# Optimization experiments

Measured on AMD Instinct MI355X. Metric: run time of the kernel, lower is better.

Reference implementation:

```python
import jax, jax.numpy as jnp
import numpy as np

N, L, D = 256, 512, 512


def _attention(x, W_in, W_out, apply_tanh):
    # x: [N, L, D]; 'general' attention: project query, score against context (=x)
    q = jnp.einsum('bld,ed->ble', x, W_in)          # [N, L, D]
    scores = jnp.einsum('bld,bmd->blm', q, x)       # [N, L, L]
    w = jax.nn.softmax(scores, axis=-1)             # softmax over keys
    mix = jnp.einsum('blm,bmd->bld', w, x)          # [N, L, D]
    comb = jnp.concatenate([mix, q], axis=-1)       # [N, L, 2D]
    out = jnp.einsum('blc,dc->bld', comb, W_out)    # Linear(2D, D), no bias
    return jnp.tanh(out) if apply_tanh else out


def setup_inputs() -> dict:
    key = jax.random.key(0)
    k1, k2, k3, k4, k5 = jax.random.split(key, 5)
    s = 0.02
    return {
        'embeddings': jax.random.normal(k1, (N, L, D), dtype=jnp.float32),
        'W_in1': jax.random.normal(k2, (D, D), dtype=jnp.float32) * s,
        'W_out1': jax.random.normal(k3, (D, 2 * D), dtype=jnp.float32) * s,
        'W_in2': jax.random.normal(k4, (D, D), dtype=jnp.float32) * s,
        'W_out2': jax.random.normal(k5, (D, 2 * D), dtype=jnp.float32) * s,
    }


def reference(embeddings, W_in1, W_out1, W_in2, W_out2):
    x = _attention(embeddings, W_in1, W_out1, apply_tanh=True)   # block 1 (tanh)
    x = _attention(x, W_in2, W_out2, apply_tanh=False)           # block 2 (no tanh)
    # transpose(1,2) + avg_pool1d over full length == mean over L
    pooled = jnp.mean(x, axis=1)                                  # [N, D]
    return pooled.reshape(pooled.shape[0], -1, 1, 1)              # [N, D, 1, 1]
```

## Files before the change

### kernel.cpp

```cpp
#include <hip/hip_runtime.h>
#include <cstdint>
#include <cstddef>

typedef uint16_t u16;
typedef __attribute__((ext_vector_type(8))) short bf16x8;
typedef __attribute__((ext_vector_type(4))) float f32x4;
typedef __attribute__((ext_vector_type(4))) uint16_t u16x4;

#define GLOBAL_AS(p) (const __attribute__((address_space(1))) void*)(p)
#define LDS_AS(p)    (__attribute__((address_space(3))) void*)(p)

__device__ __forceinline__ u16 f2b(float f){
  uint32_t u = __float_as_uint(f);
  u += 0x7fff + ((u >> 16) & 1);
  return (u16)(u >> 16);
}
__device__ __forceinline__ float b2f(u16 h){
  return __uint_as_float(((uint32_t)h) << 16);
}

__global__ void cvt_bf16_kernel(const float* __restrict__ src, u16* __restrict__ dst, int n){
  int i = (blockIdx.x * 256 + threadIdx.x) * 4;
  if (i >= n) return;
  float4 f = *(const float4*)(src + i);
  u16x4 o; o.x = f2b(f.x); o.y = f2b(f.y); o.z = f2b(f.z); o.w = f2b(f.w);
  *(u16x4*)(dst + i) = o;
}

__global__ void cvtT_kernel(const float* __restrict__ src, u16* __restrict__ x, u16* __restrict__ xT){
  __shared__ u16 tile[64][68];
  size_t b = blockIdx.y;
  int t = blockIdx.x;
  int r0 = (t >> 3) * 64, c0 = (t & 7) * 64;
  const float* s = src + b * 262144;
  u16* dx = x + b * 262144;
  u16* dT = xT + b * 262144;
  int tx = threadIdx.x & 63, ty = threadIdx.x >> 6;
  #pragma unroll
  for (int k = 0; k < 16; k++){
    int r = ty * 16 + k;
    u16 v = f2b(s[(size_t)(r0 + r) * 512 + c0 + tx]);
    dx[(size_t)(r0 + r) * 512 + c0 + tx] = v;
    tile[r][tx] = v;
  }
  __syncthreads();
  #pragma unroll
  for (int k = 0; k < 16; k++){
    int c = ty * 16 + k;
    dT[(size_t)(c0 + c) * 512 + r0 + tx] = tile[tx][c];
  }
}

__global__ void transpose512_kernel(const u16* __restrict__ src, u16* __restrict__ dst){
  __shared__ u16 tile[64][68];
  size_t b = blockIdx.y;
  int t = blockIdx.x;
  int r0 = (t >> 3) * 64, c0 = (t & 7) * 64;
  const u16* s = src + b * 262144;
  u16* d = dst + b * 262144;
  int tx = threadIdx.x & 63, ty = threadIdx.x >> 6;
  #pragma unroll
  for (int k = 0; k < 16; k++){
    int r = ty * 16 + k;
    tile[r][tx] = s[(size_t)(r0 + r) * 512 + c0 + tx];
  }
  __syncthreads();
  #pragma unroll
  for (int k = 0; k < 16; k++){
    int c = ty * 16 + k;
    d[(size_t)(c0 + c) * 512 + r0 + tx] = tile[tx][c];
  }
}

__global__ __launch_bounds__(512, 2) void attn_kernel(
    const u16* __restrict__ q, const u16* __restrict__ x, const u16* __restrict__ xT,
    u16* __restrict__ mix, int batPerXcd)
{
  __shared__ __align__(16) u16 U[64 * 520];
  __shared__ __align__(16) u16 Bx[512 * 32];
  __shared__ float stats[2][64][8];
  const int64_t E = 262144;
  int id = blockIdx.x;
  int tile = (id >> 3) & 7;
  int64_t bat = (int64_t)(id & 7) * batPerXcd + (id >> 6);
  q += bat * E; x += bat * E; xT += bat * E; mix += bat * E;
  int m0 = tile * 64;
  int tid = threadIdx.x, lane = tid & 63, w = tid >> 6;
  int fr = lane & 15, qd = lane >> 4, fq = qd * 8;

  #pragma unroll
  for (int c = 0; c < 8; c++){
    int id2 = c * 512 + tid;
    int row = id2 >> 6, cb = id2 & 63;
    *(bf16x8*)&U[row * 520 + cb * 8] =
        *(const bf16x8*)(q + (size_t)(m0 + row) * 512 + cb * 8);
  }

  f32x4 acc[4][4];
  #pragma unroll
  for (int i = 0; i < 4; i++)
    #pragma unroll
    for (int j = 0; j < 4; j++) acc[i][j] = (f32x4){0.f, 0.f, 0.f, 0.f};

  for (int k0 = 0; k0 < 512; k0 += 32){
    #pragma unroll
    for (int s = 0; s < 4; s++){
      const u16* g = x + (size_t)(s * 128 + (tid >> 2)) * 512 + k0 + (tid & 3) * 8;
      __builtin_amdgcn_global_load_lds(GLOBAL_AS(g), LDS_AS(&Bx[s * 4096 + tid * 8]), 16, 0, 0);
    }
    __syncthreads();
    bf16x8 af[4], bfr[4];
    #pragma unroll
    for (int i = 0; i < 4; i++) af[i]  = *(const bf16x8*)&U[(i * 16 + fr) * 520 + k0 + fq];
    #pragma unroll
    for (int j = 0; j < 4; j++) bfr[j] = *(const bf16x8*)&Bx[(w * 64 + j * 16 + fr) * 32 + fq];
    #pragma unroll
    for (int i = 0; i < 4; i++)
      #pragma unroll
      for (int j = 0; j < 4; j++)
        acc[i][j] = __builtin_amdgcn_mfma_f32_16x16x32_bf16(af[i], bfr[j], acc[i][j], 0, 0, 0);
    __syncthreads();
  }

  float inv[4][4];
  #pragma unroll
  for (int i = 0; i < 4; i++)
    #pragma unroll
    for (int r = 0; r < 4; r++){
      float m = acc[i][0][r];
      #pragma unroll
      for (int j = 1; j < 4; j++) m = fmaxf(m, acc[i][j][r]);
      #pragma unroll
      for (int o = 1; o <= 8; o <<= 1) m = fmaxf(m, __shfl_xor(m, o));
      if (fr == 0) stats[0][i * 16 + qd * 4 + r][w] = m;
    }
  __syncthreads();
  #pragma unroll
  for (int i = 0; i < 4; i++)
    #pragma unroll
    for (int r = 0; r < 4; r++){
      int row = i * 16 + qd * 4 + r;
      float m = stats[0][row][0];
      #pragma unroll
      for (int t = 1; t < 8; t++) m = fmaxf(m, stats[0][row][t]);
      float s = 0.f;
      #pragma unroll
      for (int j = 0; j < 4; j++){
        float e = __expf(acc[i][j][r] - m);
        acc[i][j][r] = e; s += e;
      }
      #pragma unroll
      for (int o = 1; o <= 8; o <<= 1) s += __shfl_xor(s, o);
      if (fr == 0) stats[1][row][w] = s;
    }
  __syncthreads();
  #pragma unroll
  for (int i = 0; i < 4; i++)
    #pragma unroll
    for (int r = 0; r < 4; r++){
      int row = i * 16 + qd * 4 + r;
      float s = stats[1][row][0];
      #pragma unroll
      for (int t = 1; t < 8; t++) s += stats[1][row][t];
      inv[i][r] = 1.0f / s;
    }
  #pragma unroll
  for (int i = 0; i < 4; i++)
    #pragma unroll
    for (int r = 0; r < 4; r++)
      #pragma unroll
      for (int j = 0; j < 4; j++){
        int row = i * 16 + qd * 4 + r;
        int col = w * 64 + j * 16 + fr;
        uint32_t mine = f2b(acc[i][j][r] * inv[i][r]);
        uint32_t oth = (uint32_t)__shfl_xor((int)mine, 1);
        if (!(fr & 1)) *(uint32_t*)&U[row * 520 + col] = mine | (oth << 16);
      }
  __syncthreads();

  #pragma unroll
  for (int i = 0; i < 4; i++)
    #pragma unroll
    for (int j = 0; j < 4; j++) acc[i][j] = (f32x4){0.f, 0.f, 0.f, 0.f};
  for (int k0 = 0; k0 < 512; k0 += 32){
    #pragma unroll
    for (int s = 0; s < 4; s++){
      const u16* g = xT + (size_t)(s * 128 + (tid >> 2)) * 512 + k0 + (tid & 3) * 8;
      __builtin_amdgcn_global_load_lds(GLOBAL_AS(g), LDS_AS(&Bx[s * 4096 + tid * 8]), 16, 0, 0);
    }
    __syncthreads();
    bf16x8 af[4], bfr[4];
    #pragma unroll
    for (int i = 0; i < 4; i++) af[i]  = *(const bf16x8*)&U[(i * 16 + fr) * 520 + k0 + fq];
    #pragma unroll
    for (int j = 0; j < 4; j++) bfr[j] = *(const bf16x8*)&Bx[(w * 64 + j * 16 + fr) * 32 + fq];
    #pragma unroll
    for (int i = 0; i < 4; i++)
      #pragma unroll
      for (int j = 0; j < 4; j++)
        acc[i][j] = __builtin_amdgcn_mfma_f32_16x16x32_bf16(af[i], bfr[j], acc[i][j], 0, 0, 0);
    __syncthreads();
  }
  #pragma unroll
  for (int i = 0; i < 4; i++)
    #pragma unroll
    for (int j = 0; j < 4; j++)
      #pragma unroll
      for (int r = 0; r < 4; r++)
        mix[(size_t)(m0 + i * 16 + qd * 4 + r) * 512 + w * 64 + j * 16 + fr] =
            f2b(acc[i][j][r]);
}

template<bool SPLIT, bool TANH, bool POOL, typename CT>
__global__ __launch_bounds__(256, 2) void gemm_bt_kernel(
    const u16* __restrict__ A0, const u16* __restrict__ A1,
    const u16* __restrict__ B, CT* __restrict__ C,
    int K, int ldb, int64_t aBatch, int64_t bBatch, int64_t cBatch,
    float* __restrict__ poolOut, int b0)
{
  __shared__ __align__(16) u16 As[128 * 32];
  __shared__ __align__(16) u16 Bs[128 * 32];
  int64_t bat = blockIdx.y;
  int m0 = (blockIdx.x & 3) * 128, n0 = (blockIdx.x >> 2) * 128;
  A0 += bat * aBatch;
  if (SPLIT) A1 += bat * aBatch;
  B += bat * bBatch;
  if (!POOL) C += bat * cBatch;
  int tid = threadIdx.x, lane = tid & 63;
  int w = tid >> 6;
  int wm = (w >> 1) * 64, wn = (w & 1) * 64;
  f32x4 acc[4][4];
  #pragma unroll
  for (int i = 0; i < 4; i++)
    #pragma unroll
    for (int j = 0; j < 4; j++) acc[i][j] = (f32x4){0.f, 0.f, 0.f, 0.f};

  int sRow = tid >> 2, sCol = (tid & 3) * 8;
  int fr = lane & 15, fq = (lane >> 4) * 8;

  for (int k0 = 0; k0 < K; k0 += 32){
    const u16* Ap = A0; int kk = k0;
    if (SPLIT && k0 >= 512){ Ap = A1; kk = k0 - 512; }
    const u16* ga = Ap + (size_t)(m0 + sRow) * 512 + kk + sCol;
    const u16* gb = B  + (size_t)(n0 + sRow) * ldb + k0 + sCol;
    __builtin_amdgcn_global_load_lds(GLOBAL_AS(ga),                    LDS_AS(&As[tid * 8]),        16, 0, 0);
    __builtin_amdgcn_global_load_lds(GLOBAL_AS(ga + (size_t)64 * 512), LDS_AS(&As[2048 + tid * 8]), 16, 0, 0);
    __builtin_amdgcn_global_load_lds(GLOBAL_AS(gb),                    LDS_AS(&Bs[tid * 8]),        16, 0, 0);
    __builtin_amdgcn_global_load_lds(GLOBAL_AS(gb + (size_t)64 * ldb), LDS_AS(&Bs[2048 + tid * 8]), 16, 0, 0);
    __syncthreads();
    bf16x8 af[4], bfr[4];
    #pragma unroll
    for (int i = 0; i < 4; i++) af[i]  = *(const bf16x8*)&As[(wm + i * 16 + fr) * 32 + fq];
    #pragma unroll
    for (int j = 0; j < 4; j++) bfr[j] = *(const bf16x8*)&Bs[(wn + j * 16 + fr) * 32 + fq];
    #pragma unroll
    for (int i = 0; i < 4; i++)
      #pragma unroll
      for (int j = 0; j < 4; j++)
        acc[i][j] = __builtin_amdgcn_mfma_f32_16x16x32_bf16(af[i], bfr[j], acc[i][j], 0, 0, 0);
    __syncthreads();
  }

  if constexpr (POOL){
    #pragma unroll
    for (int j = 0; j < 4; j++){
      float p = 0.f;
      #pragma unroll
      for (int i = 0; i < 4; i++)
        #pragma unroll
        for (int r = 0; r < 4; r++) p += acc[i][j][r];
      p += __shfl_xor(p, 16);
      p += __shfl_xor(p, 32);
      if (lane < 16){
        int col = n0 + wn + j * 16 + lane;
        atomicAdd(poolOut + ((size_t)(b0) + bat) * 512 + col, p * (1.0f / 512.0f));
      }
    }
  } else {
    int cq = (lane >> 4) * 4, cc = lane & 15;
    #pragma unroll
    for (int i = 0; i < 4; i++){
      #pragma unroll
      for (int j = 0; j < 4; j++){
        #pragma unroll
        for (int r = 0; r < 4; r++){
          int row = m0 + wm + i * 16 + cq + r;
          int col = n0 + wn + j * 16 + cc;
          float v = acc[i][j][r];
          if (TANH) v = tanhf(v);
          if constexpr (sizeof(CT) == 4) C[(size_t)row * 512 + col] = v;
          else                           C[(size_t)row * 512 + col] = f2b(v);
        }
      }
    }
  }
}

extern "C" void kernel_launch(void* const* d_in, const int* in_sizes, int n_in,
                              void* d_out, int out_size, void* d_ws, size_t ws_size,
                              hipStream_t stream) {
  const float* emb   = (const float*)d_in[0];
  const float* Win1  = (const float*)d_in[1];
  const float* Wout1 = (const float*)d_in[2];
  const float* Win2  = (const float*)d_in[3];
  const float* Wout2 = (const float*)d_in[4];
  float* out = (float*)d_out;

  int CB = 256;
  while (CB > 8 && (4ull << 20) + (size_t)CB * (5ull * 524288ull) > ws_size) CB >>= 1;
  const int64_t E = 262144;

  char* wsb = (char*)d_ws;
  u16* Win1b  = (u16*)wsb;
  u16* Wout1b = Win1b + 262144;
  u16* Win2b  = Wout1b + 524288;
  u16* Wout2b = Win2b + 262144;
  u16* base = (u16*)(wsb + (4 << 20));
  u16* Ar = base;
  u16* Br = base + (size_t)CB * E;
  u16* Cr = base + 2 * (size_t)CB * E;
  u16* Dr = base + 3 * (size_t)CB * E;
  u16* Fr = base + 4 * (size_t)CB * E;

  hipMemsetAsync(d_out, 0, (size_t)out_size * sizeof(float), stream);

  cvt_bf16_kernel<<<256, 256, 0, stream>>>(Win1,  Win1b,  262144);
  cvt_bf16_kernel<<<512, 256, 0, stream>>>(Wout1, Wout1b, 524288);
  cvt_bf16_kernel<<<256, 256, 0, stream>>>(Win2,  Win2b,  262144);
  cvt_bf16_kernel<<<512, 256, 0, stream>>>(Wout2, Wout2b, 524288);

  dim3 gg(16, CB);
  dim3 gt(64, CB);
  int nAttnBlocks = CB * 8;
  int batPerXcd = CB / 8;

  for (int c = 0; c < 256 / CB; c++){
    const float* embc = emb + (size_t)c * CB * 262144;
    int b0 = c * CB;

    cvtT_kernel<<<gt, 256, 0, stream>>>(embc, Ar, Cr);
    gemm_bt_kernel<false,false,false,u16><<<gg, 256, 0, stream>>>(
        Ar, nullptr, Win1b, Br, 512, 512, E, 0, E, nullptr, 0);
    attn_kernel<<<nAttnBlocks, 512, 0, stream>>>(Br, Ar, Cr, Fr, batPerXcd);
    gemm_bt_kernel<true,true,false,u16><<<gg, 256, 0, stream>>>(
        Fr, Br, Wout1b, Dr, 1024, 1024, E, 0, E, nullptr, 0);

    transpose512_kernel<<<gt, 256, 0, stream>>>(Dr, Cr);
    gemm_bt_kernel<false,false,false,u16><<<gg, 256, 0, stream>>>(
        Dr, nullptr, Win2b, Ar, 512, 512, E, 0, E, nullptr, 0);
    attn_kernel<<<nAttnBlocks, 512, 0, stream>>>(Ar, Dr, Cr, Fr, batPerXcd);
    gemm_bt_kernel<true,false,true,u16><<<gg, 256, 0, stream>>>(
        Fr, Ar, Wout2b, (u16*)nullptr, 1024, 1024, E, 0, 0, out, b0);
  }
}
```

Baseline: 1.850 ms.

## Double-buffer LDS tiles to overlap global loads with MFMA in attention and GEMM

```diff
diff --git a/kernel.cpp b/kernel.cpp
--- a/kernel.cpp
+++ b/kernel.cpp
@@ -9,6 +9,17 @@
 
 #define GLOBAL_AS(p) (const __attribute__((address_space(1))) void*)(p)
 #define LDS_AS(p)    (__attribute__((address_space(3))) void*)(p)
+
+__device__ __forceinline__ void wait_all_bar(){
+  asm volatile("s_waitcnt vmcnt(0) lgkmcnt(0)" ::: "memory");
+  __builtin_amdgcn_s_barrier();
+  asm volatile("" ::: "memory");
+}
+__device__ __forceinline__ void wait_lgkm_bar(){
+  asm volatile("s_waitcnt lgkmcnt(0)" ::: "memory");
+  __builtin_amdgcn_s_barrier();
+  asm volatile("" ::: "memory");
+}
 
 __device__ __forceinline__ u16 f2b(float f){
   uint32_t u = __float_as_uint(f);
@@ -77,7 +88,7 @@
     u16* __restrict__ mix, int batPerXcd)
 {
   __shared__ __align__(16) u16 U[64 * 520];
-  __shared__ __align__(16) u16 Bx[512 * 32];
+  __shared__ __align__(16) u16 Bx[2][512 * 32];
   __shared__ float stats[2][64][8];
   const int64_t E = 262144;
   int id = blockIdx.x;
@@ -88,6 +99,16 @@
   int tid = threadIdx.x, lane = tid & 63, w = tid >> 6;
   int fr = lane & 15, qd = lane >> 4, fq = qd * 8;
 
+  auto stage = [&](const u16* __restrict__ src, int buf, int k0){
+    #pragma unroll
+    for (int s = 0; s < 4; s++){
+      const u16* g = src + (size_t)(s * 128 + (tid >> 2)) * 512 + k0 + (tid & 3) * 8;
+      __builtin_amdgcn_global_load_lds(GLOBAL_AS(g), LDS_AS(&Bx[buf][s * 4096 + tid * 8]), 16, 0, 0);
+    }
+  };
+
+  stage(x, 0, 0);
+
   #pragma unroll
   for (int c = 0; c < 8; c++){
     int id2 = c * 512 + tid;
@@ -102,25 +123,25 @@
     #pragma unroll
     for (int j = 0; j < 4; j++) acc[i][j] = (f32x4){0.f, 0.f, 0.f, 0.f};
 
-  for (int k0 = 0; k0 < 512; k0 += 32){
-    #pragma unroll
-    for (int s = 0; s < 4; s++){
-      const u16* g = x + (size_t)(s * 128 + (tid >> 2)) * 512 + k0 + (tid & 3) * 8;
-      __builtin_amdgcn_global_load_lds(GLOBAL_AS(g), LDS_AS(&Bx[s * 4096 + tid * 8]), 16, 0, 0);
-    }
-    __syncthreads();
+  wait_all_bar();
+
+  for (int it = 0; it < 16; ++it){
+    if (it < 15) stage(x, (it + 1) & 1, (it + 1) * 32);
+    int k0 = it * 32;
     bf16x8 af[4], bfr[4];
     #pragma unroll
     for (int i = 0; i < 4; i++) af[i]  = *(const bf16x8*)&U[(i * 16 + fr) * 520 + k0 + fq];
     #pragma unroll
-    for (int j = 0; j < 4; j++) bfr[j] = *(const bf16x8*)&Bx[(w * 64 + j * 16 + fr) * 32 + fq];
+    for (int j = 0; j < 4; j++) bfr[j] = *(const bf16x8*)&Bx[it & 1][(w * 64 + j * 16 + fr) * 32 + fq];
     #pragma unroll
     for (int i = 0; i < 4; i++)
       #pragma unroll
       for (int j = 0; j < 4; j++)
         acc[i][j] = __builtin_amdgcn_mfma_f32_16x16x32_bf16(af[i], bfr[j], acc[i][j], 0, 0, 0);
-    __syncthreads();
-  }
+    wait_all_bar();
+  }
+
+  stage(xT, 0, 0);
 
   float inv[4][4];
   #pragma unroll
@@ -134,7 +155,7 @@
       for (int o = 1; o <= 8; o <<= 1) m = fmaxf(m, __shfl_xor(m, o));
       if (fr == 0) stats[0][i * 16 + qd * 4 + r][w] = m;
     }
-  __syncthreads();
+  wait_lgkm_bar();
   #pragma unroll
   for (int i = 0; i < 4; i++)
     #pragma unroll
@@ -153,7 +174,7 @@
       for (int o = 1; o <= 8; o <<= 1) s += __shfl_xor(s, o);
       if (fr == 0) stats[1][row][w] = s;
     }
-  __syncthreads();
+  wait_lgkm_bar();
   #pragma unroll
   for (int i = 0; i < 4; i++)
     #pragma unroll
@@ -176,30 +197,26 @@
         uint32_t oth = (uint32_t)__shfl_xor((int)mine, 1);
         if (!(fr & 1)) *(uint32_t*)&U[row * 520 + col] = mine | (oth << 16);
       }
-  __syncthreads();
+  wait_all_bar();
 
   #pragma unroll
   for (int i = 0; i < 4; i++)
     #pragma unroll
     for (int j = 0; j < 4; j++) acc[i][j] = (f32x4){0.f, 0.f, 0.f, 0.f};
-  for (int k0 = 0; k0 < 512; k0 += 32){
-    #pragma unroll
-    for (int s = 0; s < 4; s++){
-      const u16* g = xT + (size_t)(s * 128 + (tid >> 2)) * 512 + k0 + (tid & 3) * 8;
-      __builtin_amdgcn_global_load_lds(GLOBAL_AS(g), LDS_AS(&Bx[s * 4096 + tid * 8]), 16, 0, 0);
-    }
-    __syncthreads();
+  for (int it = 0; it < 16; ++it){
+    if (it < 15) stage(xT, (it + 1) & 1, (it + 1) * 32);
+    int k0 = it * 32;
     bf16x8 af[4], bfr[4];
     #pragma unroll
     for (int i = 0; i < 4; i++) af[i]  = *(const bf16x8*)&U[(i * 16 + fr) * 520 + k0 + fq];
     #pragma unroll
-    for (int j = 0; j < 4; j++) bfr[j] = *(const bf16x8*)&Bx[(w * 64 + j * 16 + fr) * 32 + fq];
+    for (int j = 0; j < 4; j++) bfr[j] = *(const bf16x8*)&Bx[it & 1][(w * 64 + j * 16 + fr) * 32 + fq];
     #pragma unroll
     for (int i = 0; i < 4; i++)
       #pragma unroll
       for (int j = 0; j < 4; j++)
         acc[i][j] = __builtin_amdgcn_mfma_f32_16x16x32_bf16(af[i], bfr[j], acc[i][j], 0, 0, 0);
-    __syncthreads();
+    wait_all_bar();
   }
   #pragma unroll
   for (int i = 0; i < 4; i++)
@@ -218,8 +235,8 @@
     int K, int ldb, int64_t aBatch, int64_t bBatch, int64_t cBatch,
     float* __restrict__ poolOut, int b0)
 {
-  __shared__ __align__(16) u16 As[128 * 32];
-  __shared__ __align__(16) u16 Bs[128 * 32];
+  __shared__ __align__(16) u16 As[2][128 * 32];
+  __shared__ __align__(16) u16 Bs[2][128 * 32];
   int64_t bat = blockIdx.y;
   int m0 = (blockIdx.x & 3) * 128, n0 = (blockIdx.x >> 2) * 128;
   A0 += bat * aBatch;
@@ -238,27 +255,34 @@
   int sRow = tid >> 2, sCol = (tid & 3) * 8;
   int fr = lane & 15, fq = (lane >> 4) * 8;
 
-  for (int k0 = 0; k0 < K; k0 += 32){
+  auto stageG = [&](int buf, int k0){
     const u16* Ap = A0; int kk = k0;
     if (SPLIT && k0 >= 512){ Ap = A1; kk = k0 - 512; }
     const u16* ga = Ap + (size_t)(m0 + sRow) * 512 + kk + sCol;
     const u16* gb = B  + (size_t)(n0 + sRow) * ldb + k0 + sCol;
-    __builtin_amdgcn_global_load_lds(GLOBAL_AS(ga),                    LDS_AS(&As[tid * 8]),        16, 0, 0);
-    __builtin_amdgcn_global_load_lds(GLOBAL_AS(ga + (size_t)64 * 512), LDS_AS(&As[2048 + tid * 8]), 16, 0, 0);
-    __builtin_amdgcn_global_load_lds(GLOBAL_AS(gb),                    LDS_AS(&Bs[tid * 8]),        16, 0, 0);
-    __builtin_amdgcn_global_load_lds(GLOBAL_AS(gb + (size_t)64 * ldb), LDS_AS(&Bs[2048 + tid * 8]), 16, 0, 0);
-    __syncthreads();
+    __builtin_amdgcn_global_load_lds(GLOBAL_AS(ga),                    LDS_AS(&As[buf][tid * 8]),        16, 0, 0);
+    __builtin_amdgcn_global_load_lds(GLOBAL_AS(ga + (size_t)64 * 512), LDS_AS(&As[buf][2048 + tid * 8]), 16, 0, 0);
+    __builtin_amdgcn_global_load_lds(GLOBAL_AS(gb),                    LDS_AS(&Bs[buf][tid * 8]),        16, 0, 0);
+    __builtin_amdgcn_global_load_lds(GLOBAL_AS(gb + (size_t)64 * ldb), LDS_AS(&Bs[buf][2048 + tid * 8]), 16, 0, 0);
+  };
+
+  stageG(0, 0);
+  wait_all_bar();
+
+  int nIt = K >> 5;
+  for (int it = 0; it < nIt; ++it){
+    if (it + 1 < nIt) stageG((it + 1) & 1, (it + 1) * 32);
     bf16x8 af[4], bfr[4];
     #pragma unroll
-    for (int i = 0; i < 4; i++) af[i]  = *(const bf16x8*)&As[(wm + i * 16 + fr) * 32 + fq];
-    #pragma unroll
-    for (int j = 0; j < 4; j++) bfr[j] = *(const bf16x8*)&Bs[(wn + j * 16 + fr) * 32 + fq];
+    for (int i = 0; i < 4; i++) af[i]  = *(const bf16x8*)&As[it & 1][(wm + i * 16 + fr) * 32 + fq];
+    #pragma unroll
+    for (int j = 0; j < 4; j++) bfr[j] = *(const bf16x8*)&Bs[it & 1][(wn + j * 16 + fr) * 32 + fq];
     #pragma unroll
     for (int i = 0; i < 4; i++)
       #pragma unroll
       for (int j = 0; j < 4; j++)
         acc[i][j] = __builtin_amdgcn_mfma_f32_16x16x32_bf16(af[i], bfr[j], acc[i][j], 0, 0, 0);
-    __syncthreads();
+    wait_all_bar();
   }
 
   if constexpr (POOL){
```

Measured after the change: 1.754 ms. 5.2% less time.

## Stream B operands from global into registers with 4-deep prefetch, drop LDS staging

Applied to the files above, without the earlier changes.

```diff
diff --git a/kernel.cpp b/kernel.cpp
--- a/kernel.cpp
+++ b/kernel.cpp
@@ -10,13 +10,21 @@
 #define GLOBAL_AS(p) (const __attribute__((address_space(1))) void*)(p)
 #define LDS_AS(p)    (__attribute__((address_space(3))) void*)(p)
 
+__device__ __forceinline__ void bar_vm0(){
+  asm volatile("s_waitcnt vmcnt(0)" ::: "memory");
+  __builtin_amdgcn_s_barrier();
+  asm volatile("" ::: "memory");
+}
+__device__ __forceinline__ void bar_lgkm(){
+  asm volatile("s_waitcnt lgkmcnt(0)" ::: "memory");
+  __builtin_amdgcn_s_barrier();
+  asm volatile("" ::: "memory");
+}
+
 __device__ __forceinline__ u16 f2b(float f){
   uint32_t u = __float_as_uint(f);
   u += 0x7fff + ((u >> 16) & 1);
   return (u16)(u >> 16);
-}
-__device__ __forceinline__ float b2f(u16 h){
-  return __uint_as_float(((uint32_t)h) << 16);
 }
 
 __global__ void cvt_bf16_kernel(const float* __restrict__ src, u16* __restrict__ dst, int n){
@@ -77,7 +85,6 @@
     u16* __restrict__ mix, int batPerXcd)
 {
   __shared__ __align__(16) u16 U[64 * 520];
-  __shared__ __align__(16) u16 Bx[512 * 32];
   __shared__ float stats[2][64][8];
   const int64_t E = 262144;
   int id = blockIdx.x;
@@ -90,11 +97,23 @@
 
   #pragma unroll
   for (int c = 0; c < 8; c++){
-    int id2 = c * 512 + tid;
-    int row = id2 >> 6, cb = id2 & 63;
-    *(bf16x8*)&U[row * 520 + cb * 8] =
-        *(const bf16x8*)(q + (size_t)(m0 + row) * 512 + cb * 8);
-  }
+    int row = c * 8 + w;
+    __builtin_amdgcn_global_load_lds(GLOBAL_AS(q + (size_t)(m0 + row) * 512 + lane * 8),
+                                     LDS_AS(&U[row * 520 + lane * 8]), 16, 0, 0);
+  }
+
+  int vo[4];
+  #pragma unroll
+  for (int j = 0; j < 4; j++) vo[j] = (w * 64 + j * 16 + fr) * 512 + fq;
+
+  bf16x8 rb[4][4];
+  #pragma unroll
+  for (int t = 0; t < 4; t++)
+    #pragma unroll
+    for (int j = 0; j < 4; j++)
+      rb[t][j] = *(const bf16x8*)(x + vo[j] + t * 32);
+
+  bar_vm0();
 
   f32x4 acc[4][4];
   #pragma unroll
@@ -102,24 +121,24 @@
     #pragma unroll
     for (int j = 0; j < 4; j++) acc[i][j] = (f32x4){0.f, 0.f, 0.f, 0.f};
 
-  for (int k0 = 0; k0 < 512; k0 += 32){
-    #pragma unroll
-    for (int s = 0; s < 4; s++){
-      const u16* g = x + (size_t)(s * 128 + (tid >> 2)) * 512 + k0 + (tid & 3) * 8;
-      __builtin_amdgcn_global_load_lds(GLOBAL_AS(g), LDS_AS(&Bx[s * 4096 + tid * 8]), 16, 0, 0);
-    }
-    __syncthreads();
-    bf16x8 af[4], bfr[4];
-    #pragma unroll
-    for (int i = 0; i < 4; i++) af[i]  = *(const bf16x8*)&U[(i * 16 + fr) * 520 + k0 + fq];
-    #pragma unroll
-    for (int j = 0; j < 4; j++) bfr[j] = *(const bf16x8*)&Bx[(w * 64 + j * 16 + fr) * 32 + fq];
+  #pragma unroll
+  for (int it = 0; it < 16; ++it){
+    int k0 = it * 32;
+    bf16x8 af[4];
+    #pragma unroll
+    for (int i = 0; i < 4; i++) af[i] = *(const bf16x8*)&U[(i * 16 + fr) * 520 + k0 + fq];
     #pragma unroll
     for (int i = 0; i < 4; i++)
       #pragma unroll
       for (int j = 0; j < 4; j++)
-        acc[i][j] = __builtin_amdgcn_mfma_f32_16x16x32_bf16(af[i], bfr[j], acc[i][j], 0, 0, 0);
-    __syncthreads();
+        acc[i][j] = __builtin_amdgcn_mfma_f32_16x16x32_bf16(af[i], rb[it & 3][j], acc[i][j], 0, 0, 0);
+    if (it < 12){
+      #pragma unroll
+      for (int j = 0; j < 4; j++) rb[it & 3][j] = *(const bf16x8*)(x + vo[j] + (it + 4) * 32);
+    } else {
+      #pragma unroll
+      for (int j = 0; j < 4; j++) rb[it & 3][j] = *(const bf16x8*)(xT + vo[j] + (it - 12) * 32);
+    }
   }
 
   float inv[4][4];
@@ -134,7 +153,7 @@
       for (int o = 1; o <= 8; o <<= 1) m = fmaxf(m, __shfl_xor(m, o));
       if (fr == 0) stats[0][i * 16 + qd * 4 + r][w] = m;
     }
-  __syncthreads();
+  bar_lgkm();
   #pragma unroll
   for (int i = 0; i < 4; i++)
     #pragma unroll
@@ -153,7 +172,7 @@
       for (int o = 1; o <= 8; o <<= 1) s += __shfl_xor(s, o);
       if (fr == 0) stats[1][row][w] = s;
     }
-  __syncthreads();
+  bar_lgkm();
   #pragma unroll
   for (int i = 0; i < 4; i++)
     #pragma unroll
@@ -176,30 +195,27 @@
         uint32_t oth = (uint32_t)__shfl_xor((int)mine, 1);
         if (!(fr & 1)) *(uint32_t*)&U[row * 520 + col] = mine | (oth << 16);
       }
-  __syncthreads();
+  bar_lgkm();
 
   #pragma unroll
   for (int i = 0; i < 4; i++)
     #pragma unroll
     for (int j = 0; j < 4; j++) acc[i][j] = (f32x4){0.f, 0.f, 0.f, 0.f};
-  for (int k0 = 0; k0 < 512; k0 += 32){
-    #pragma unroll
-    for (int s = 0; s < 4; s++){
-      const u16* g = xT + (size_t)(s * 128 + (tid >> 2)) * 512 + k0 + (tid & 3) * 8;
-      __builtin_amdgcn_global_load_lds(GLOBAL_AS(g), LDS_AS(&Bx[s * 4096 + tid * 8]), 16, 0, 0);
-    }
-    __syncthreads();
-    bf16x8 af[4], bfr[4];
-    #pragma unroll
-    for (int i = 0; i < 4; i++) af[i]  = *(const bf16x8*)&U[(i * 16 + fr) * 520 + k0 + fq];
-    #pragma unroll
-    for (int j = 0; j < 4; j++) bfr[j] = *(const bf16x8*)&Bx[(w * 64 + j * 16 + fr) * 32 + fq];
+  #pragma unroll
+  for (int it = 0; it < 16; ++it){
+    int k0 = it * 32;
+    bf16x8 af[4];
+    #pragma unroll
+    for (int i = 0; i < 4; i++) af[i] = *(const bf16x8*)&U[(i * 16 + fr) * 520 + k0 + fq];
     #pragma unroll
     for (int i = 0; i < 4; i++)
       #pragma unroll
       for (int j = 0; j < 4; j++)
-        acc[i][j] = __builtin_amdgcn_mfma_f32_16x16x32_bf16(af[i], bfr[j], acc[i][j], 0, 0, 0);
-    __syncthreads();
+        acc[i][j] = __builtin_amdgcn_mfma_f32_16x16x32_bf16(af[i], rb[it & 3][j], acc[i][j], 0, 0, 0);
+    if (it < 12){
+      #pragma unroll
+      for (int j = 0; j < 4; j++) rb[it & 3][j] = *(const bf16x8*)(xT + vo[j] + (it + 4) * 32);
+    }
   }
   #pragma unroll
   for (int i = 0; i < 4; i++)
```

Result: faster. 1.800 ms (-2.7%).
